# Performance work log

Measured on AMD Instinct MI355X. Metric: run time of the kernel, lower is better.

Reference implementation:

```python
import jax, jax.numpy as jnp
import numpy as np

EPS = 1e-5

def _layernorm(x, g, b):
    m = jnp.mean(x, axis=-1, keepdims=True)
    v = jnp.mean(jnp.square(x - m), axis=-1, keepdims=True)
    return (x - m) * jax.lax.rsqrt(v + EPS) * g + b

def setup_inputs() -> dict:
    key = jax.random.key(0)
    B, S, D, H = 2, 2048, 1024, 16
    F = 4 * D
    ks = jax.random.split(key, 12)
    s = 1.0 / np.sqrt(D)
    inp = {
        "x": jax.random.normal(ks[0], (B, S, D), dtype=jnp.float32),
        "mask": jnp.ones((B, S), dtype=jnp.int32),
        "wq": jax.random.normal(ks[1], (D, D), dtype=jnp.float32) * s,
        "bq": jnp.zeros((D,), jnp.float32),
        "wk": jax.random.normal(ks[2], (D, D), dtype=jnp.float32) * s,
        "bk": jnp.zeros((D,), jnp.float32),
        "wv": jax.random.normal(ks[3], (D, D), dtype=jnp.float32) * s,
        "bv": jnp.zeros((D,), jnp.float32),
        "wo": jax.random.normal(ks[4], (D, D), dtype=jnp.float32) * s,
        "bo": jnp.zeros((D,), jnp.float32),
        "g1": jnp.ones((D,), jnp.float32),
        "be1": jnp.zeros((D,), jnp.float32),
        "g2": jnp.ones((D,), jnp.float32),
        "be2": jnp.zeros((D,), jnp.float32),
        "w1": jax.random.normal(ks[5], (D, F), dtype=jnp.float32) * s,
        "bf1": jnp.zeros((F,), jnp.float32),
        "w2": jax.random.normal(ks[6], (F, D), dtype=jnp.float32) * (1.0 / np.sqrt(F)),
        "bf2": jnp.zeros((D,), jnp.float32),
    }
    return inp

def reference(x, mask, wq, bq, wk, bk, wv, bv, wo, bo, g1, be1, g2, be2, w1, bf1, w2, bf2):
    B, S, D = x.shape
    H = 16
    hd = D // H
    residual = x
    xn = _layernorm(x, g1, be1)
    q = (xn @ wq + bq).reshape(B, S, H, hd).transpose(0, 2, 1, 3)  # [B,H,S,hd]
    k = (xn @ wk + bk).reshape(B, S, H, hd).transpose(0, 2, 1, 3)
    v = (xn @ wv + bv).reshape(B, S, H, hd).transpose(0, 2, 1, 3)
    scores = jnp.einsum('bhqd,bhkd->bhqk', q, k) / np.sqrt(hd)  # [B,H,S,S]
    scores = jnp.where(mask[:, None, None, :] == 0, jnp.float32(-1e9), scores)
    attn = jax.nn.softmax(scores, axis=-1)
    attended = jnp.einsum('bhqk,bhkd->bhqd', attn, v)
    attended = attended.transpose(0, 2, 1, 3).reshape(B, S, D)
    x = residual + (attended @ wo + bo)
    residual = x
    xn = _layernorm(x, g2, be2)
    ff = jax.nn.relu(xn @ w1 + bf1) @ w2 + bf2
    return residual + ff
```

## Files before the change

kernel.cpp:

```cpp
#include <hip/hip_runtime.h>
#include <hip/hip_bf16.h>


using bf16 = __hip_bfloat16;
typedef short bf16x8 __attribute__((ext_vector_type(8)));
typedef short bf16x4v __attribute__((ext_vector_type(4)));
typedef float f32x4 __attribute__((ext_vector_type(4)));

#if defined(__has_builtin)
#  if __has_builtin(__builtin_amdgcn_mfma_f32_16x16x16bf16_1k)
#    define HAVE_MFMA_K16 1
#  endif
#  if __has_builtin(__builtin_amdgcn_exp2f)
#    define EXP2F(x) __builtin_amdgcn_exp2f(x)
#  endif
#endif
#ifndef EXP2F
#  define EXP2F(x) __expf(0.6931471805599453f * (x))
#endif

__device__ __forceinline__ float toF(float v) { return v; }
__device__ __forceinline__ float toF(bf16 v) { return __bfloat162float(v); }
__device__ __forceinline__ void storeF(float* p, float v) { *p = v; }
__device__ __forceinline__ void storeF(bf16* p, float v) { *p = __float2bfloat16(v); }

__device__ __forceinline__ float waveReduceSum(float v) {
    #pragma unroll
    for (int o = 32; o > 0; o >>= 1) v += __shfl_down(v, o, 64);
    return v;
}

__device__ __forceinline__ void async16(const bf16* g, bf16* l) {
    __builtin_amdgcn_global_load_lds(
        (const __attribute__((address_space(1))) unsigned int*)g,
        (__attribute__((address_space(3))) unsigned int*)l,
        16, 0, 0);
}

__device__ __forceinline__ unsigned short bf16bits(float x) {
    union { bf16 h; unsigned short u; } e; e.h = __float2bfloat16(x);
    return e.u;
}

__global__ __launch_bounds__(256) void transpose_all(
        const float* __restrict__ wq, const float* __restrict__ wk,
        const float* __restrict__ wv, const float* __restrict__ wo,
        const float* __restrict__ w1, const float* __restrict__ w2,
        bf16* __restrict__ wqkvT, bf16* __restrict__ woT,
        bf16* __restrict__ w1T, bf16* __restrict__ w2T) {
    __shared__ float t[32][33];
    const int tI = blockIdx.x;
    const float* in; bf16* outT; int R, C, tl;
    if (tI < 4096) {
        const int seg = tI >> 10; tl = tI & 1023; R = 1024; C = 1024;
        in = (seg == 0) ? wq : (seg == 1) ? wk : (seg == 2) ? wv : wo;
        outT = (seg == 3) ? woT : wqkvT + (size_t)seg * 1024 * 1024;
    } else if (tI < 8192) {
        tl = tI - 4096; in = w1; outT = w1T; R = 1024; C = 4096;
    } else {
        tl = tI - 8192; in = w2; outT = w2T; R = 4096; C = 1024;
    }
    const int tc = C >> 5;
    const int c0 = (tl % tc) * 32, r0 = (tl / tc) * 32;
    const int lx = threadIdx.x & 31, ly = threadIdx.x >> 5;
    #pragma unroll
    for (int i = 0; i < 32; i += 8)
        t[ly + i][lx] = in[(size_t)(r0 + ly + i) * C + c0 + lx];
    __syncthreads();
    #pragma unroll
    for (int i = 0; i < 32; i += 8)
        outT[(size_t)(c0 + ly + i) * R + r0 + lx] = __float2bfloat16(t[lx][ly + i]);
}

template <typename InT>
__global__ __launch_bounds__(256) void ln_kernel(const InT* __restrict__ x,
                                                 const float* __restrict__ g,
                                                 const float* __restrict__ b,
                                                 bf16* __restrict__ out, int D) {
    const int row = blockIdx.x;
    const InT* xr = x + (size_t)row * D;
    float s = 0.f, s2 = 0.f;
    for (int i = threadIdx.x; i < D; i += 256) {
        float v = toF(xr[i]);
        s += v; s2 += v * v;
    }
    __shared__ float ws[4], ws2[4];
    int lane = threadIdx.x & 63, wid = threadIdx.x >> 6;
    s = waveReduceSum(s); s2 = waveReduceSum(s2);
    if (lane == 0) { ws[wid] = s; ws2[wid] = s2; }
    __syncthreads();
    float ts = ws[0] + ws[1] + ws[2] + ws[3];
    float ts2 = ws2[0] + ws2[1] + ws2[2] + ws2[3];
    float mean = ts / D;
    float var = ts2 / D - mean * mean;
    float rstd = rsqrtf(var + 1e-5f);
    bf16* outr = out + (size_t)row * D;
    for (int i = threadIdx.x; i < D; i += 256) {
        float v = (toF(xr[i]) - mean) * rstd * g[i] + b[i];
        outr[i] = __float2bfloat16(v);
    }
}

template <int BM, typename OutT, typename ResidT, bool RELU, bool HAS_RESID, bool BIAS3>
__global__ __launch_bounds__(256) void gemm_mfma(const bf16* __restrict__ A,
                                                 const bf16* __restrict__ BT,
                                                 const float* __restrict__ bias,
                                                 const float* __restrict__ biasK,
                                                 const float* __restrict__ biasV,
                                                 const ResidT* __restrict__ resid,
                                                 OutT* __restrict__ C,
                                                 int M, int N, int K) {
    constexpr int BK = 64;
    constexpr int MI = BM / 32;
    constexpr int AROWS = BM / 4;
    constexpr int ASEC = AROWS / 8;
    __shared__ bf16 As[BM][BK];
    __shared__ bf16 Bs[128][BK];
    const int tid = threadIdx.x, lane = tid & 63, wid = tid >> 6;
    const int m0 = blockIdx.y * BM, n0 = blockIdx.x * 128;
    const int wm = (BM == 128) ? (wid >> 1) * 64 : (wid & 1) * 32;
    const int wn = (BM == 128) ? (wid & 1) * 64 : (wid >> 1) * 64;

    f32x4 acc[MI][4] = {};

    const int srow = lane >> 3;
    const int scol = ((lane & 7) ^ srow) * 8;
    const bf16* Abase = A + (size_t)(m0 + wid * AROWS + srow) * K + scol;
    const bf16* Bbase = BT + (size_t)(n0 + wid * 32 + srow) * K + scol;

    const int fr = lane & 15;
    const int kg = lane >> 4;

    for (int k0 = 0; k0 < K; k0 += BK) {
        #pragma unroll
        for (int s = 0; s < ASEC; ++s)
            async16(Abase + (size_t)(s * 8) * K + k0, &As[wid * AROWS + s * 8][0]);
        #pragma unroll
        for (int s = 0; s < 4; ++s)
            async16(Bbase + (size_t)(s * 8) * K + k0, &Bs[wid * 32 + s * 8][0]);
        __syncthreads();

        #pragma unroll
        for (int ks = 0; ks < 2; ++ks) {
            const int pc = ((ks * 4 + kg) ^ (fr & 7)) * 16;
            bf16x8 aF[MI], bF[4];
            #pragma unroll
            for (int i = 0; i < MI; ++i)
                aF[i] = *(const bf16x8*)((const char*)&As[0][0]
                         + (size_t)(wm + i * 16 + fr) * 128 + pc);
            #pragma unroll
            for (int j = 0; j < 4; ++j)
                bF[j] = *(const bf16x8*)((const char*)&Bs[0][0]
                         + (size_t)(wn + j * 16 + fr) * 128 + pc);
            #pragma unroll
            for (int i = 0; i < MI; ++i)
                #pragma unroll
                for (int j = 0; j < 4; ++j)
                    acc[i][j] = __builtin_amdgcn_mfma_f32_16x16x32_bf16(
                        aF[i], bF[j], acc[i][j], 0, 0, 0);
        }
        __syncthreads();
    }

    const int col_l = lane & 15, row_l = (lane >> 4) * 4;
    #pragma unroll
    for (int j = 0; j < 4; ++j) {
        const int col = n0 + wn + j * 16 + col_l;
        float bvv;
        if (BIAS3) {
            const float* bp = (col < 1024) ? bias : ((col < 2048) ? biasK : biasV);
            bvv = bp[col & 1023];
        } else {
            bvv = bias[col];
        }
        #pragma unroll
        for (int i = 0; i < MI; ++i) {
            #pragma unroll
            for (int r = 0; r < 4; ++r) {
                const int row = m0 + wm + i * 16 + row_l + r;
                float v = acc[i][j][r] + bvv;
                if (RELU) v = fmaxf(v, 0.f);
                if (HAS_RESID) v += toF(resid[(size_t)row * N + col]);
                storeF(&C[(size_t)row * N + col], v);
            }
        }
    }
}

#if HAVE_MFMA_K16
__global__ __launch_bounds__(256) void attn_mfma(const bf16* __restrict__ qkv,
                                                 const int* __restrict__ mask,
                                                 bf16* __restrict__ outp,
                                                 int B, int S, int LD) {
    const int q0 = blockIdx.x * 128;
    const int h = blockIdx.y, b = blockIdx.z;
    const int Do = 1024;
    const int tid = threadIdx.x, lane = tid & 63, wid = tid >> 6;
    const int n = lane & 15, kg = lane >> 4;

    __shared__ bf16 Ks[2][64][66];
    __shared__ bf16 Vt[2][64][68];
    __shared__ float Mskf[2][64];
    __shared__ int sAny[2];

    const float QSCALE = 0.125f * 1.4426950408889634f;
    bf16x8 qf[2][2];
    #pragma unroll
    for (int u = 0; u < 2; ++u) {
        const bf16* qp = qkv + ((size_t)(b * S + q0 + wid * 32 + u * 16 + n)) * LD + h * 64 + kg * 8;
        union { uint4 uu; bf16x8 v; unsigned short s[8]; } c[2];
        c[0].uu = *(const uint4*)qp;
        c[1].uu = *(const uint4*)(qp + 32);
        #pragma unroll
        for (int t = 0; t < 2; ++t) {
            #pragma unroll
            for (int i = 0; i < 8; ++i) {
                union { float f; unsigned int u2; } d;
                d.u2 = ((unsigned int)c[t].s[i]) << 16;
                c[t].s[i] = bf16bits(d.f * QSCALE);
            }
            qf[u][t] = c[t].v;
        }
    }

    f32x4 acc[2][4] = {};
    float m[2] = {-1e30f, -1e30f}, l[2] = {0.f, 0.f};

    const int sr = tid >> 2, sc = (tid & 3) * 16;
    const int jp = tid & 31, dg = (tid >> 5) * 8;
    const bf16* kbase = qkv + (size_t)(b * S) * LD + 1024 + h * 64;
    const bf16* vbase = qkv + (size_t)(b * S) * LD + 2048 + h * 64;

    uint4 ka, kc, vau, vcu;
    int mz = 0;

    {
        const bf16* kp = kbase + (size_t)sr * LD + sc;
        ka = *(const uint4*)kp;
        kc = *(const uint4*)(kp + 8);
        const bf16* vp = vbase + (size_t)(2 * jp) * LD + dg;
        vau = *(const uint4*)vp;
        vcu = *(const uint4*)(vp + LD);
        if (tid < 64) mz = (mask[b * S + tid] == 0);
    }

    const int NT = S / 64;
    for (int t = 0; t < NT; ++t) {
        const int cur = t & 1;

        {
            uint* kd = (uint*)((char*)&Ks[cur][0][0] + sr * 132 + sc * 2);
            kd[0] = ka.x; kd[1] = ka.y; kd[2] = ka.z; kd[3] = ka.w;
            kd[4] = kc.x; kd[5] = kc.y; kd[6] = kc.z; kd[7] = kc.w;

            union { uint4 u4; unsigned short s[8]; } va, vc;
            va.u4 = vau; vc.u4 = vcu;
            #pragma unroll
            for (int i = 0; i < 8; ++i) {
                unsigned int pk = (unsigned int)va.s[i] | ((unsigned int)vc.s[i] << 16);
                *(unsigned int*)((char*)&Vt[cur][0][0] + (size_t)(dg + i) * 136 + jp * 4) = pk;
            }
            if (tid < 64) {
                Mskf[cur][tid] = mz ? -1e9f : 0.f;
                unsigned long long bl = __ballot(mz);
                if (tid == 0) sAny[cur] = (bl != 0ull) ? 1 : 0;
            }
        }
        __syncthreads();

        if (t + 1 < NT) {
            const int j0 = (t + 1) * 64;
            const bf16* kp = kbase + (size_t)(j0 + sr) * LD + sc;
            ka = *(const uint4*)kp;
            kc = *(const uint4*)(kp + 8);
            const bf16* vp = vbase + (size_t)(j0 + 2 * jp) * LD + dg;
            vau = *(const uint4*)vp;
            vcu = *(const uint4*)(vp + LD);
            if (tid < 64) mz = (mask[b * S + j0 + tid] == 0);
        }

        f32x4 st[2][4] = {};
        #pragma unroll
        for (int ks = 0; ks < 2; ++ks) {
            #pragma unroll
            for (int jt = 0; jt < 4; ++jt) {
                union { uint u[4]; bf16x8 v; } kf;
                const uint* bp = (const uint*)((const char*)&Ks[cur][0][0]
                                 + (size_t)(jt * 16 + n) * 132 + ks * 64 + kg * 16);
                kf.u[0] = bp[0]; kf.u[1] = bp[1]; kf.u[2] = bp[2]; kf.u[3] = bp[3];
                st[0][jt] = __builtin_amdgcn_mfma_f32_16x16x32_bf16(kf.v, qf[0][ks], st[0][jt], 0, 0, 0);
                st[1][jt] = __builtin_amdgcn_mfma_f32_16x16x32_bf16(kf.v, qf[1][ks], st[1][jt], 0, 0, 0);
            }
        }

        if (sAny[cur]) {
            #pragma unroll
            for (int u = 0; u < 2; ++u) {
                #pragma unroll
                for (int jt = 0; jt < 4; ++jt) {
                    f32x4 mb = *(const f32x4*)&Mskf[cur][jt * 16 + kg * 4];
                    #pragma unroll
                    for (int r = 0; r < 4; ++r) st[u][jt][r] += mb[r];
                }
            }
        }

        float mx0 = st[0][0][0], mx1 = st[1][0][0];
        #pragma unroll
        for (int jt = 0; jt < 4; ++jt) {
            #pragma unroll
            for (int r = 0; r < 4; ++r) {
                mx0 = fmaxf(mx0, st[0][jt][r]);
                mx1 = fmaxf(mx1, st[1][jt][r]);
            }
        }
        mx0 = fmaxf(mx0, __shfl_xor(mx0, 16, 64));
        mx0 = fmaxf(mx0, __shfl_xor(mx0, 32, 64));
        mx1 = fmaxf(mx1, __shfl_xor(mx1, 16, 64));
        mx1 = fmaxf(mx1, __shfl_xor(mx1, 32, 64));

        if (__any((mx0 > m[0] + 8.f) || (mx1 > m[1] + 8.f))) {
            float mxa[2] = {mx0, mx1};
            #pragma unroll
            for (int u = 0; u < 2; ++u) {
                float newm = fmaxf(m[u], mxa[u]);
                float alpha = EXP2F(m[u] - newm);
                m[u] = newm;
                l[u] *= alpha;
                #pragma unroll
                for (int dt = 0; dt < 4; ++dt)
                    #pragma unroll
                    for (int r = 0; r < 4; ++r) acc[u][dt][r] *= alpha;
            }
        }

        bf16x4v pf[2][4];
        #pragma unroll
        for (int u = 0; u < 2; ++u) {
            float ls = 0.f;
            #pragma unroll
            for (int jt = 0; jt < 4; ++jt) {
                union { unsigned short s[4]; bf16x4v v; } pk;
                #pragma unroll
                for (int r = 0; r < 4; ++r) {
                    union { float f; unsigned int u2; } p;
                    p.f = EXP2F(st[u][jt][r] - m[u]);
                    p.u2 &= 0xffff0000u;
                    ls += p.f;
                    pk.s[r] = (unsigned short)(p.u2 >> 16);
                }
                pf[u][jt] = pk.v;
            }
            ls += __shfl_xor(ls, 16, 64);
            ls += __shfl_xor(ls, 32, 64);
            l[u] += ls;
        }

        #pragma unroll
        for (int jt = 0; jt < 4; ++jt) {
            #pragma unroll
            for (int dt = 0; dt < 4; ++dt) {
                union { uint u[2]; bf16x4v v; } vf;
                const uint* vpp = (const uint*)((const char*)&Vt[cur][0][0]
                                  + (size_t)(dt * 16 + n) * 136 + jt * 32 + kg * 8);
                vf.u[0] = vpp[0]; vf.u[1] = vpp[1];
                acc[0][dt] = __builtin_amdgcn_mfma_f32_16x16x16bf16_1k(vf.v, pf[0][jt], acc[0][dt], 0, 0, 0);
                acc[1][dt] = __builtin_amdgcn_mfma_f32_16x16x16bf16_1k(vf.v, pf[1][jt], acc[1][dt], 0, 0, 0);
            }
        }
    }

    #pragma unroll
    for (int u = 0; u < 2; ++u) {
        float inv = (l[u] > 0.f) ? (1.f / l[u]) : 0.f;
        bf16* op = outp + ((size_t)(b * S + q0 + wid * 32 + u * 16 + n)) * Do + h * 64;
        #pragma unroll
        for (int dt = 0; dt < 4; ++dt) {
            union { unsigned short s[4]; uint2 u2; } w;
            #pragma unroll
            for (int r = 0; r < 4; ++r) w.s[r] = bf16bits(acc[u][dt][r] * inv);
            *(uint2*)(op + dt * 16 + kg * 4) = w.u2;
        }
    }
}
#else
__global__ __launch_bounds__(256) void attn_mfma(const bf16* __restrict__ qkv,
                                                 const int* __restrict__ mask,
                                                 bf16* __restrict__ outp,
                                                 int B, int S, int LD) {
    const int h = blockIdx.y, b = blockIdx.z;
    const int Do = 1024;
    const int tid = threadIdx.x, lane = tid & 63, wid = tid >> 6;
    const int n = lane & 15, kg = lane >> 4;

    __shared__ bf16 Ks[64][66];
    __shared__ bf16 Vt[64][66];
    __shared__ bf16 Plds[4][16][66];
    __shared__ int  Msk[64];

    for (int half = 0; half < 2; ++half) {
        const int q0 = blockIdx.x * 128 + half * 64;
        __syncthreads();

        bf16x8 qf[2];
        {
            const bf16* qp = qkv + ((size_t)(b * S + q0 + wid * 16 + n)) * LD + h * 64 + kg * 8;
            union { uint4 u; bf16x8 v; } c0, c1;
            c0.u = *(const uint4*)qp;
            c1.u = *(const uint4*)(qp + 32);
            qf[0] = c0.v; qf[1] = c1.v;
        }

        f32x4 acc_o[4] = {};
        float m_r[4] = {-1e30f, -1e30f, -1e30f, -1e30f};
        float l_r[4] = {0.f, 0.f, 0.f, 0.f};

        const int sr = tid >> 2;
        const int sc = (tid & 3) * 16;
        const bf16* kbase = qkv + (size_t)(b * S) * LD + 1024 + h * 64;
        const bf16* vbase = qkv + (size_t)(b * S) * LD + 2048 + h * 64;

        for (int j0 = 0; j0 < S; j0 += 64) {
            __syncthreads();
            {
                const bf16* kp = kbase + (size_t)(j0 + sr) * LD + sc;
                uint4 ka = *(const uint4*)kp;
                uint4 kbv = *(const uint4*)(kp + 8);
                uint* kd = (uint*)((char*)&Ks[0][0] + sr * 132 + sc * 2);
                kd[0] = ka.x; kd[1] = ka.y; kd[2] = ka.z; kd[3] = ka.w;
                kd[4] = kbv.x; kd[5] = kbv.y; kd[6] = kbv.z; kd[7] = kbv.w;

                const bf16* vp = vbase + (size_t)(j0 + sr) * LD + sc;
                union { uint4 u[2]; unsigned short s[16]; } vv;
                vv.u[0] = *(const uint4*)vp;
                vv.u[1] = *(const uint4*)(vp + 8);
                #pragma unroll
                for (int i = 0; i < 16; ++i)
                    *((unsigned short*)((char*)&Vt[0][0] + (size_t)(sc + i) * 132 + sr * 2)) = vv.s[i];

                if (tid < 64) Msk[tid] = mask[b * S + j0 + tid];
            }
            __syncthreads();

            f32x4 st[4] = {};
            #pragma unroll
            for (int ks = 0; ks < 2; ++ks) {
                #pragma unroll
                for (int jt = 0; jt < 4; ++jt) {
                    union { uint u[4]; bf16x8 v; } bf;
                    const uint* bp = (const uint*)((const char*)&Ks[0][0]
                                     + (size_t)(jt * 16 + n) * 132 + ks * 64 + kg * 16);
                    bf.u[0] = bp[0]; bf.u[1] = bp[1]; bf.u[2] = bp[2]; bf.u[3] = bp[3];
                    st[jt] = __builtin_amdgcn_mfma_f32_16x16x32_bf16(qf[ks], bf.v, st[jt], 0, 0, 0);
                }
            }

            int mk[4];
            #pragma unroll
            for (int jt = 0; jt < 4; ++jt) mk[jt] = Msk[jt * 16 + n];

            #pragma unroll
            for (int r = 0; r < 4; ++r) {
                float mx = -1e30f;
                #pragma unroll
                for (int jt = 0; jt < 4; ++jt) {
                    float s = st[jt][r] * 0.125f;
                    if (mk[jt] == 0) s = -1e9f;
                    st[jt][r] = s;
                    mx = fmaxf(mx, s);
                }
                #pragma unroll
                for (int o = 1; o < 16; o <<= 1) mx = fmaxf(mx, __shfl_xor(mx, o, 64));
                float newm = fmaxf(m_r[r], mx);
                float alpha = __expf(m_r[r] - newm);
                m_r[r] = newm;
                float ls = 0.f;
                #pragma unroll
                for (int jt = 0; jt < 4; ++jt) {
                    float p = __expf(st[jt][r] - newm);
                    ls += p;
                    Plds[wid][kg * 4 + r][jt * 16 + n] = __float2bfloat16(p);
                }
                #pragma unroll
                for (int o = 1; o < 16; o <<= 1) ls += __shfl_xor(ls, o, 64);
                l_r[r] = l_r[r] * alpha + ls;
                #pragma unroll
                for (int dt = 0; dt < 4; ++dt) acc_o[dt][r] *= alpha;
            }

            __asm__ volatile("s_waitcnt lgkmcnt(0)" ::: "memory");

            #pragma unroll
            for (int ks = 0; ks < 2; ++ks) {
                union { uint u[4]; bf16x8 v; } af;
                const uint* ap = (const uint*)((const char*)&Plds[wid][0][0]
                                 + (size_t)n * 132 + ks * 64 + kg * 16);
                af.u[0] = ap[0]; af.u[1] = ap[1]; af.u[2] = ap[2]; af.u[3] = ap[3];
                #pragma unroll
                for (int dt = 0; dt < 4; ++dt) {
                    union { uint u[4]; bf16x8 v; } bf;
                    const uint* bp = (const uint*)((const char*)&Vt[0][0]
                                     + (size_t)(dt * 16 + n) * 132 + ks * 64 + kg * 16);
                    bf.u[0] = bp[0]; bf.u[1] = bp[1]; bf.u[2] = bp[2]; bf.u[3] = bp[3];
                    acc_o[dt] = __builtin_amdgcn_mfma_f32_16x16x32_bf16(af.v, bf.v, acc_o[dt], 0, 0, 0);
                }
            }
        }

        #pragma unroll
        for (int r = 0; r < 4; ++r) {
            float inv = (l_r[r] > 0.f) ? (1.f / l_r[r]) : 0.f;
            bf16* op = outp + ((size_t)(b * S + q0 + wid * 16 + kg * 4 + r)) * Do + h * 64 + n;
            #pragma unroll
            for (int dt = 0; dt < 4; ++dt)
                op[dt * 16] = __float2bfloat16(acc_o[dt][r] * inv);
        }
    }
}
#endif

extern "C" void kernel_launch(void* const* d_in, const int* in_sizes, int n_in,
                              void* d_out, int out_size, void* d_ws, size_t ws_size,
                              hipStream_t stream) {
    const int B = 2, S = 2048, D = 1024, H = 16, F = 4096;
    const int M = B * S;

    const float* x   = (const float*)d_in[0];
    const int*   mask= (const int*)  d_in[1];
    const float* wq  = (const float*)d_in[2];
    const float* bq  = (const float*)d_in[3];
    const float* wk  = (const float*)d_in[4];
    const float* bk  = (const float*)d_in[5];
    const float* wv  = (const float*)d_in[6];
    const float* bv  = (const float*)d_in[7];
    const float* wo  = (const float*)d_in[8];
    const float* bo  = (const float*)d_in[9];
    const float* g1  = (const float*)d_in[10];
    const float* be1 = (const float*)d_in[11];
    const float* g2  = (const float*)d_in[12];
    const float* be2 = (const float*)d_in[13];
    const float* w1  = (const float*)d_in[14];
    const float* bf1 = (const float*)d_in[15];
    const float* w2  = (const float*)d_in[16];
    const float* bf2 = (const float*)d_in[17];
    float* out = (float*)d_out;

    char* ws = (char*)d_ws;
    const size_t MB = 1024 * 1024;
    bf16* wqkvT = (bf16*)(ws + 0 * MB);
    bf16* woT   = (bf16*)(ws + 6 * MB);
    bf16* w1T   = (bf16*)(ws + 8 * MB);
    bf16* w2T   = (bf16*)(ws + 16 * MB);
    bf16* xn    = (bf16*)(ws + 24 * MB);
    bf16* qkv   = (bf16*)(ws + 32 * MB);
    bf16* att   = xn;

    const bool fullM = (ws_size >= 64 * MB);

    transpose_all<<<12288, 256, 0, stream>>>(wq, wk, wv, wo, w1, w2,
                                             wqkvT, woT, w1T, w2T);

    ln_kernel<float><<<M, 256, 0, stream>>>(x, g1, be1, xn, D);

    gemm_mfma<128, bf16, float, false, false, true><<<dim3(3072 / 128, M / 128), 256, 0, stream>>>(
        xn, wqkvT, bq, bk, bv, (const float*)nullptr, qkv, M, 3072, D);

    attn_mfma<<<dim3(S / 128, H, B), 256, 0, stream>>>(qkv, mask, att, B, S, 3072);

    gemm_mfma<64, float, float, false, true, false><<<dim3(D / 128, M / 64), 256, 0, stream>>>(
        att, woT, bo, nullptr, nullptr, x, out, M, D, D);

    if (fullM) {
        bf16* hid = (bf16*)(ws + 24 * MB);
        bf16* xn2 = (bf16*)(ws + 56 * MB);
        ln_kernel<float><<<M, 256, 0, stream>>>(out, g2, be2, xn2, D);
        gemm_mfma<128, bf16, float, true, false, false><<<dim3(F / 128, M / 128), 256, 0, stream>>>(
            xn2, w1T, bf1, nullptr, nullptr, (const float*)nullptr, hid, M, F, D);
        gemm_mfma<64, float, float, false, true, false><<<dim3(D / 128, M / 64), 256, 0, stream>>>(
            hid, w2T, bf2, nullptr, nullptr, out, out, M, D, F);
    } else {
        bf16* xn2 = (bf16*)(ws + 32 * MB);
        bf16* hid = (bf16*)(ws + 40 * MB);
        const int CH = 2048;
        ln_kernel<float><<<M, 256, 0, stream>>>(out, g2, be2, xn2, D);
        for (int c = 0; c < M / CH; ++c) {
            const size_t roff = (size_t)c * CH;
            gemm_mfma<128, bf16, float, true, false, false><<<dim3(F / 128, CH / 128), 256, 0, stream>>>(
                xn2 + roff * D, w1T, bf1, nullptr, nullptr, (const float*)nullptr, hid, CH, F, D);
            gemm_mfma<64, float, float, false, true, false><<<dim3(D / 128, CH / 64), 256, 0, stream>>>(
                hid, w2T, bf2, nullptr, nullptr, out + roff * D, out + roff * D, CH, D, F);
        }
    }
}
```

Measured before the change: 392.2 us.

## Split attention KV sequence across two wave groups and merge partial softmax

The attention kernel now launches 512 threads per block, split into two groups of four waves. Each group processes alternating 64-key tiles for the same 128 queries with its own double-buffered LDS slots. At the end, the partial max, sum and output of group 1 are merged into group 0 through shared memory. The aim is to add parallelism and hide latency, since the grid has only 512 blocks. The cost is about 70KB of LDS per block, which limits occupancy, plus an extra merge step.

```diff
diff --git a/kernel.cpp b/kernel.cpp
--- a/kernel.cpp
+++ b/kernel.cpp
@@ -188,26 +188,30 @@
 }
 
 #if HAVE_MFMA_K16
-__global__ __launch_bounds__(256) void attn_mfma(const bf16* __restrict__ qkv,
-                                                 const int* __restrict__ mask,
-                                                 bf16* __restrict__ outp,
-                                                 int B, int S, int LD) {
+__global__ __launch_bounds__(512, 4) void attn_mfma(const bf16* __restrict__ qkv,
+                                                    const int* __restrict__ mask,
+                                                    bf16* __restrict__ outp,
+                                                    int B, int S, int LD) {
     const int q0 = blockIdx.x * 128;
     const int h = blockIdx.y, b = blockIdx.z;
     const int Do = 1024;
     const int tid = threadIdx.x, lane = tid & 63, wid = tid >> 6;
+    const int g = wid >> 2;
+    const int wl = wid & 3;
+    const int stid = tid & 255;
     const int n = lane & 15, kg = lane >> 4;
 
-    __shared__ bf16 Ks[2][64][66];
-    __shared__ bf16 Vt[2][64][68];
-    __shared__ float Mskf[2][64];
-    __shared__ int sAny[2];
+    __shared__ __align__(16) char smem[70672];
+    bf16* KsBase = (bf16*)smem;
+    bf16* VtBase = (bf16*)(smem + 33792);
+    float* MskfP = (float*)(smem + 68608);
+    int* sAnyP   = (int*)(smem + 70656);
 
     const float QSCALE = 0.125f * 1.4426950408889634f;
     bf16x8 qf[2][2];
     #pragma unroll
     for (int u = 0; u < 2; ++u) {
-        const bf16* qp = qkv + ((size_t)(b * S + q0 + wid * 32 + u * 16 + n)) * LD + h * 64 + kg * 8;
+        const bf16* qp = qkv + ((size_t)(b * S + q0 + wl * 32 + u * 16 + n)) * LD + h * 64 + kg * 8;
         union { uint4 uu; bf16x8 v; unsigned short s[8]; } c[2];
         c[0].uu = *(const uint4*)qp;
         c[1].uu = *(const uint4*)(qp + 32);
@@ -226,8 +230,8 @@
     f32x4 acc[2][4] = {};
     float m[2] = {-1e30f, -1e30f}, l[2] = {0.f, 0.f};
 
-    const int sr = tid >> 2, sc = (tid & 3) * 16;
-    const int jp = tid & 31, dg = (tid >> 5) * 8;
+    const int sr = stid >> 2, sc = (stid & 3) * 16;
+    const int jp = stid & 31, dg = (stid >> 5) * 8;
     const bf16* kbase = qkv + (size_t)(b * S) * LD + 1024 + h * 64;
     const bf16* vbase = qkv + (size_t)(b * S) * LD + 2048 + h * 64;
 
@@ -235,21 +239,25 @@
     int mz = 0;
 
     {
-        const bf16* kp = kbase + (size_t)sr * LD + sc;
+        const int j0 = g * 64;
+        const bf16* kp = kbase + (size_t)(j0 + sr) * LD + sc;
         ka = *(const uint4*)kp;
         kc = *(const uint4*)(kp + 8);
-        const bf16* vp = vbase + (size_t)(2 * jp) * LD + dg;
+        const bf16* vp = vbase + (size_t)(j0 + 2 * jp) * LD + dg;
         vau = *(const uint4*)vp;
         vcu = *(const uint4*)(vp + LD);
-        if (tid < 64) mz = (mask[b * S + tid] == 0);
+        if (stid < 64) mz = (mask[b * S + j0 + stid] == 0);
     }
 
     const int NT = S / 64;
-    for (int t = 0; t < NT; ++t) {
-        const int cur = t & 1;
+    for (int it = 0; it < NT / 2; ++it) {
+        const int cur = it & 1;
+        const int slot = g * 2 + cur;
+        bf16* ksb = KsBase + slot * (64 * 66);
+        bf16* vtb = VtBase + slot * (64 * 68);
 
         {
-            uint* kd = (uint*)((char*)&Ks[cur][0][0] + sr * 132 + sc * 2);
+            uint* kd = (uint*)((char*)ksb + sr * 132 + sc * 2);
             kd[0] = ka.x; kd[1] = ka.y; kd[2] = ka.z; kd[3] = ka.w;
             kd[4] = kc.x; kd[5] = kc.y; kd[6] = kc.z; kd[7] = kc.w;
 
@@ -258,25 +266,28 @@
             #pragma unroll
             for (int i = 0; i < 8; ++i) {
                 unsigned int pk = (unsigned int)va.s[i] | ((unsigned int)vc.s[i] << 16);
-                *(unsigned int*)((char*)&Vt[cur][0][0] + (size_t)(dg + i) * 136 + jp * 4) = pk;
-            }
-            if (tid < 64) {
-                Mskf[cur][tid] = mz ? -1e9f : 0.f;
+                *(unsigned int*)((char*)vtb + (size_t)(dg + i) * 136 + jp * 4) = pk;
+            }
+            if (stid < 64) {
+                MskfP[slot * 64 + stid] = mz ? -1e9f : 0.f;
                 unsigned long long bl = __ballot(mz);
-                if (tid == 0) sAny[cur] = (bl != 0ull) ? 1 : 0;
+                if (stid == 0) sAnyP[slot] = (bl != 0ull) ? 1 : 0;
             }
         }
         __syncthreads();
 
-        if (t + 1 < NT) {
-            const int j0 = (t + 1) * 64;
-            const bf16* kp = kbase + (size_t)(j0 + sr) * LD + sc;
-            ka = *(const uint4*)kp;
-            kc = *(const uint4*)(kp + 8);
-            const bf16* vp = vbase + (size_t)(j0 + 2 * jp) * LD + dg;
-            vau = *(const uint4*)vp;
-            vcu = *(const uint4*)(vp + LD);
-            if (tid < 64) mz = (mask[b * S + j0 + tid] == 0);
+        {
+            const int tg2 = 2 * (it + 1) + g;
+            if (tg2 < NT) {
+                const int j0 = tg2 * 64;
+                const bf16* kp = kbase + (size_t)(j0 + sr) * LD + sc;
+                ka = *(const uint4*)kp;
+                kc = *(const uint4*)(kp + 8);
+                const bf16* vp = vbase + (size_t)(j0 + 2 * jp) * LD + dg;
+                vau = *(const uint4*)vp;
+                vcu = *(const uint4*)(vp + LD);
+                if (stid < 64) mz = (mask[b * S + j0 + stid] == 0);
+            }
         }
 
         f32x4 st[2][4] = {};
@@ -285,7 +296,7 @@
             #pragma unroll
             for (int jt = 0; jt < 4; ++jt) {
                 union { uint u[4]; bf16x8 v; } kf;
-                const uint* bp = (const uint*)((const char*)&Ks[cur][0][0]
+                const uint* bp = (const uint*)((const char*)ksb
                                  + (size_t)(jt * 16 + n) * 132 + ks * 64 + kg * 16);
                 kf.u[0] = bp[0]; kf.u[1] = bp[1]; kf.u[2] = bp[2]; kf.u[3] = bp[3];
                 st[0][jt] = __builtin_amdgcn_mfma_f32_16x16x32_bf16(kf.v, qf[0][ks], st[0][jt], 0, 0, 0);
@@ -293,12 +304,12 @@
             }
         }
 
-        if (sAny[cur]) {
+        if (sAnyP[slot]) {
             #pragma unroll
             for (int u = 0; u < 2; ++u) {
                 #pragma unroll
                 for (int jt = 0; jt < 4; ++jt) {
-                    f32x4 mb = *(const f32x4*)&Mskf[cur][jt * 16 + kg * 4];
+                    f32x4 mb = *(const f32x4*)&MskfP[slot * 64 + jt * 16 + kg * 4];
                     #pragma unroll
                     for (int r = 0; r < 4; ++r) st[u][jt][r] += mb[r];
                 }
@@ -361,7 +372,7 @@
             #pragma unroll
             for (int dt = 0; dt < 4; ++dt) {
                 union { uint u[2]; bf16x4v v; } vf;
-                const uint* vpp = (const uint*)((const char*)&Vt[cur][0][0]
+                const uint* vpp = (const uint*)((const char*)vtb
                                   + (size_t)(dt * 16 + n) * 136 + jt * 32 + kg * 8);
                 vf.u[0] = vpp[0]; vf.u[1] = vpp[1];
                 acc[0][dt] = __builtin_amdgcn_mfma_f32_16x16x16bf16_1k(vf.v, pf[0][jt], acc[0][dt], 0, 0, 0);
@@ -370,21 +381,49 @@
         }
     }
 
-    #pragma unroll
-    for (int u = 0; u < 2; ++u) {
-        float inv = (l[u] > 0.f) ? (1.f / l[u]) : 0.f;
-        bf16* op = outp + ((size_t)(b * S + q0 + wid * 32 + u * 16 + n)) * Do + h * 64;
-        #pragma unroll
-        for (int dt = 0; dt < 4; ++dt) {
-            union { unsigned short s[4]; uint2 u2; } w;
-            #pragma unroll
-            for (int r = 0; r < 4; ++r) w.s[r] = bf16bits(acc[u][dt][r] * inv);
-            *(uint2*)(op + dt * 16 + kg * 4) = w.u2;
+    __syncthreads();
+    float* po = (float*)smem;
+    float* pm = (float*)(smem + 33280);
+    float* pl = (float*)(smem + 33792);
+    if (g == 1) {
+        #pragma unroll
+        for (int u = 0; u < 2; ++u) {
+            const int ql = wl * 32 + u * 16 + n;
+            if (kg == 0) { pm[ql] = m[u]; pl[ql] = l[u]; }
+            #pragma unroll
+            for (int dt = 0; dt < 4; ++dt)
+                #pragma unroll
+                for (int r = 0; r < 4; ++r)
+                    po[ql * 65 + dt * 16 + kg * 4 + r] = acc[u][dt][r];
+        }
+    }
+    __syncthreads();
+    if (g == 0) {
+        #pragma unroll
+        for (int u = 0; u < 2; ++u) {
+            const int ql = wl * 32 + u * 16 + n;
+            float m1 = pm[ql], l1 = pl[ql];
+            float newm = fmaxf(m[u], m1);
+            float a0 = EXP2F(m[u] - newm);
+            float a1 = EXP2F(m1 - newm);
+            float lt = l[u] * a0 + l1 * a1;
+            float inv = (lt > 0.f) ? (1.f / lt) : 0.f;
+            bf16* op = outp + ((size_t)(b * S + q0 + wl * 32 + u * 16 + n)) * Do + h * 64;
+            #pragma unroll
+            for (int dt = 0; dt < 4; ++dt) {
+                union { unsigned short s[4]; uint2 u2; } w;
+                #pragma unroll
+                for (int r = 0; r < 4; ++r) {
+                    float o1 = po[ql * 65 + dt * 16 + kg * 4 + r];
+                    w.s[r] = bf16bits((acc[u][dt][r] * a0 + o1 * a1) * inv);
+                }
+                *(uint2*)(op + dt * 16 + kg * 4) = w.u2;
+            }
         }
     }
 }
 #else
-__global__ __launch_bounds__(256) void attn_mfma(const bf16* __restrict__ qkv,
+__global__ __launch_bounds__(512) void attn_mfma(const bf16* __restrict__ qkv,
                                                  const int* __restrict__ mask,
                                                  bf16* __restrict__ outp,
                                                  int B, int S, int LD) {
@@ -392,129 +431,125 @@
     const int Do = 1024;
     const int tid = threadIdx.x, lane = tid & 63, wid = tid >> 6;
     const int n = lane & 15, kg = lane >> 4;
+    const int q0 = blockIdx.x * 128;
 
     __shared__ bf16 Ks[64][66];
     __shared__ bf16 Vt[64][66];
-    __shared__ bf16 Plds[4][16][66];
+    __shared__ bf16 Plds[8][16][66];
     __shared__ int  Msk[64];
 
-    for (int half = 0; half < 2; ++half) {
-        const int q0 = blockIdx.x * 128 + half * 64;
+    bf16x8 qf[2];
+    {
+        const bf16* qp = qkv + ((size_t)(b * S + q0 + wid * 16 + n)) * LD + h * 64 + kg * 8;
+        union { uint4 u; bf16x8 v; } c0, c1;
+        c0.u = *(const uint4*)qp;
+        c1.u = *(const uint4*)(qp + 32);
+        qf[0] = c0.v; qf[1] = c1.v;
+    }
+
+    f32x4 acc_o[4] = {};
+    float m_r[4] = {-1e30f, -1e30f, -1e30f, -1e30f};
+    float l_r[4] = {0.f, 0.f, 0.f, 0.f};
+
+    const int sr = tid >> 2;
+    const int sc = (tid & 3) * 16;
+    const bf16* kbase = qkv + (size_t)(b * S) * LD + 1024 + h * 64;
+    const bf16* vbase = qkv + (size_t)(b * S) * LD + 2048 + h * 64;
+
+    for (int j0 = 0; j0 < S; j0 += 64) {
         __syncthreads();
-
-        bf16x8 qf[2];
-        {
-            const bf16* qp = qkv + ((size_t)(b * S + q0 + wid * 16 + n)) * LD + h * 64 + kg * 8;
-            union { uint4 u; bf16x8 v; } c0, c1;
-            c0.u = *(const uint4*)qp;
-            c1.u = *(const uint4*)(qp + 32);
-            qf[0] = c0.v; qf[1] = c1.v;
-        }
-
-        f32x4 acc_o[4] = {};
-        float m_r[4] = {-1e30f, -1e30f, -1e30f, -1e30f};
-        float l_r[4] = {0.f, 0.f, 0.f, 0.f};
-
-        const int sr = tid >> 2;
-        const int sc = (tid & 3) * 16;
-        const bf16* kbase = qkv + (size_t)(b * S) * LD + 1024 + h * 64;
-        const bf16* vbase = qkv + (size_t)(b * S) * LD + 2048 + h * 64;
-
-        for (int j0 = 0; j0 < S; j0 += 64) {
-            __syncthreads();
-            {
-                const bf16* kp = kbase + (size_t)(j0 + sr) * LD + sc;
-                uint4 ka = *(const uint4*)kp;
-                uint4 kbv = *(const uint4*)(kp + 8);
-                uint* kd = (uint*)((char*)&Ks[0][0] + sr * 132 + sc * 2);
-                kd[0] = ka.x; kd[1] = ka.y; kd[2] = ka.z; kd[3] = ka.w;
-                kd[4] = kbv.x; kd[5] = kbv.y; kd[6] = kbv.z; kd[7] = kbv.w;
-
-                const bf16* vp = vbase + (size_t)(j0 + sr) * LD + sc;
-                union { uint4 u[2]; unsigned short s[16]; } vv;
-                vv.u[0] = *(const uint4*)vp;
-                vv.u[1] = *(const uint4*)(vp + 8);
-                #pragma unroll
-                for (int i = 0; i < 16; ++i)
-                    *((unsigned short*)((char*)&Vt[0][0] + (size_t)(sc + i) * 132 + sr * 2)) = vv.s[i];
-
-                if (tid < 64) Msk[tid] = mask[b * S + j0 + tid];
-            }
-            __syncthreads();
-
-            f32x4 st[4] = {};
-            #pragma unroll
-            for (int ks = 0; ks < 2; ++ks) {
-                #pragma unroll
-                for (int jt = 0; jt < 4; ++jt) {
-                    union { uint u[4]; bf16x8 v; } bf;
-                    const uint* bp = (const uint*)((const char*)&Ks[0][0]
-                                     + (size_t)(jt * 16 + n) * 132 + ks * 64 + kg * 16);
-                    bf.u[0] = bp[0]; bf.u[1] = bp[1]; bf.u[2] = bp[2]; bf.u[3] = bp[3];
-                    st[jt] = __builtin_amdgcn_mfma_f32_16x16x32_bf16(qf[ks], bf.v, st[jt], 0, 0, 0);
-                }
-            }
-
-            int mk[4];
-            #pragma unroll
-            for (int jt = 0; jt < 4; ++jt) mk[jt] = Msk[jt * 16 + n];
-
-            #pragma unroll
-            for (int r = 0; r < 4; ++r) {
-                float mx = -1e30f;
-                #pragma unroll
-                for (int jt = 0; jt < 4; ++jt) {
-                    float s = st[jt][r] * 0.125f;
-                    if (mk[jt] == 0) s = -1e9f;
-                    st[jt][r] = s;
-                    mx = fmaxf(mx, s);
-                }
-                #pragma unroll
-                for (int o = 1; o < 16; o <<= 1) mx = fmaxf(mx, __shfl_xor(mx, o, 64));
-                float newm = fmaxf(m_r[r], mx);
-                float alpha = __expf(m_r[r] - newm);
-                m_r[r] = newm;
-                float ls = 0.f;
-                #pragma unroll
-                for (int jt = 0; jt < 4; ++jt) {
-                    float p = __expf(st[jt][r] - newm);
-                    ls += p;
-                    Plds[wid][kg * 4 + r][jt * 16 + n] = __float2bfloat16(p);
-                }
-                #pragma unroll
-                for (int o = 1; o < 16; o <<= 1) ls += __shfl_xor(ls, o, 64);
-                l_r[r] = l_r[r] * alpha + ls;
-                #pragma unroll
-                for (int dt = 0; dt < 4; ++dt) acc_o[dt][r] *= alpha;
-            }
-
-            __asm__ volatile("s_waitcnt lgkmcnt(0)" ::: "memory");
-
-            #pragma unroll
-            for (int ks = 0; ks < 2; ++ks) {
-                union { uint u[4]; bf16x8 v; } af;
-                const uint* ap = (const uint*)((const char*)&Plds[wid][0][0]
-                                 + (size_t)n * 132 + ks * 64 + kg * 16);
-                af.u[0] = ap[0]; af.u[1] = ap[1]; af.u[2] = ap[2]; af.u[3] = ap[3];
-                #pragma unroll
-                for (int dt = 0; dt < 4; ++dt) {
-                    union { uint u[4]; bf16x8 v; } bf;
-                    const uint* bp = (const uint*)((const char*)&Vt[0][0]
-                                     + (size_t)(dt * 16 + n) * 132 + ks * 64 + kg * 16);
-                    bf.u[0] = bp[0]; bf.u[1] = bp[1]; bf.u[2] = bp[2]; bf.u[3] = bp[3];
-                    acc_o[dt] = __builtin_amdgcn_mfma_f32_16x16x32_bf16(af.v, bf.v, acc_o[dt], 0, 0, 0);
-                }
-            }
-        }
+        if (tid < 256) {
+            const bf16* kp = kbase + (size_t)(j0 + sr) * LD + sc;
+            uint4 ka = *(const uint4*)kp;
+            uint4 kbv = *(const uint4*)(kp + 8);
+            uint* kd = (uint*)((char*)&Ks[0][0] + sr * 132 + sc * 2);
+            kd[0] = ka.x; kd[1] = ka.y; kd[2] = ka.z; kd[3] = ka.w;
+            kd[4] = kbv.x; kd[5] = kbv.y; kd[6] = kbv.z; kd[7] = kbv.w;
+
+            const bf16* vp = vbase + (size_t)(j0 + sr) * LD + sc;
+            union { uint4 u[2]; unsigned short s[16]; } vv;
+            vv.u[0] = *(const uint4*)vp;
+            vv.u[1] = *(const uint4*)(vp + 8);
+            #pragma unroll
+            for (int i = 0; i < 16; ++i)
+                *((unsigned short*)((char*)&Vt[0][0] + (size_t)(sc + i) * 132 + sr * 2)) = vv.s[i];
+
+            if (tid < 64) Msk[tid] = mask[b * S + j0 + tid];
+        }
+        __syncthreads();
+
+        f32x4 st[4] = {};
+        #pragma unroll
+        for (int ks = 0; ks < 2; ++ks) {
+            #pragma unroll
+            for (int jt = 0; jt < 4; ++jt) {
+                union { uint u[4]; bf16x8 v; } bf;
+                const uint* bp = (const uint*)((const char*)&Ks[0][0]
+                                 + (size_t)(jt * 16 + n) * 132 + ks * 64 + kg * 16);
+                bf.u[0] = bp[0]; bf.u[1] = bp[1]; bf.u[2] = bp[2]; bf.u[3] = bp[3];
+                st[jt] = __builtin_amdgcn_mfma_f32_16x16x32_bf16(qf[ks], bf.v, st[jt], 0, 0, 0);
+            }
+        }
+
+        int mk[4];
+        #pragma unroll
+        for (int jt = 0; jt < 4; ++jt) mk[jt] = Msk[jt * 16 + n];
 
         #pragma unroll
         for (int r = 0; r < 4; ++r) {
-            float inv = (l_r[r] > 0.f) ? (1.f / l_r[r]) : 0.f;
-            bf16* op = outp + ((size_t)(b * S + q0 + wid * 16 + kg * 4 + r)) * Do + h * 64 + n;
-            #pragma unroll
-            for (int dt = 0; dt < 4; ++dt)
-                op[dt * 16] = __float2bfloat16(acc_o[dt][r] * inv);
-        }
+            float mx = -1e30f;
+            #pragma unroll
+            for (int jt = 0; jt < 4; ++jt) {
+                float s = st[jt][r] * 0.125f;
+                if (mk[jt] == 0) s = -1e9f;
+                st[jt][r] = s;
+                mx = fmaxf(mx, s);
+            }
+            #pragma unroll
+            for (int o = 1; o < 16; o <<= 1) mx = fmaxf(mx, __shfl_xor(mx, o, 64));
+            float newm = fmaxf(m_r[r], mx);
+            float alpha = __expf(m_r[r] - newm);
+            m_r[r] = newm;
+            float ls = 0.f;
+            #pragma unroll
+            for (int jt = 0; jt < 4; ++jt) {
+                float p = __expf(st[jt][r] - newm);
+                ls += p;
+                Plds[wid][kg * 4 + r][jt * 16 + n] = __float2bfloat16(p);
+            }
+            #pragma unroll
+            for (int o = 1; o < 16; o <<= 1) ls += __shfl_xor(ls, o, 64);
+            l_r[r] = l_r[r] * alpha + ls;
+            #pragma unroll
+            for (int dt = 0; dt < 4; ++dt) acc_o[dt][r] *= alpha;
+        }
+
+        __asm__ volatile("s_waitcnt lgkmcnt(0)" ::: "memory");
+
+        #pragma unroll
+        for (int ks = 0; ks < 2; ++ks) {
+            union { uint u[4]; bf16x8 v; } af;
+            const uint* ap = (const uint*)((const char*)&Plds[wid][0][0]
+                             + (size_t)n * 132 + ks * 64 + kg * 16);
+            af.u[0] = ap[0]; af.u[1] = ap[1]; af.u[2] = ap[2]; af.u[3] = ap[3];
+            #pragma unroll
+            for (int dt = 0; dt < 4; ++dt) {
+                union { uint u[4]; bf16x8 v; } bf;
+                const uint* bp = (const uint*)((const char*)&Vt[0][0]
+                                 + (size_t)(dt * 16 + n) * 132 + ks * 64 + kg * 16);
+                bf.u[0] = bp[0]; bf.u[1] = bp[1]; bf.u[2] = bp[2]; bf.u[3] = bp[3];
+                acc_o[dt] = __builtin_amdgcn_mfma_f32_16x16x32_bf16(af.v, bf.v, acc_o[dt], 0, 0, 0);
+            }
+        }
+    }
+
+    #pragma unroll
+    for (int r = 0; r < 4; ++r) {
+        float inv = (l_r[r] > 0.f) ? (1.f / l_r[r]) : 0.f;
+        bf16* op = outp + ((size_t)(b * S + q0 + wid * 16 + kg * 4 + r)) * Do + h * 64 + n;
+        #pragma unroll
+        for (int dt = 0; dt < 4; ++dt)
+            op[dt * 16] = __float2bfloat16(acc_o[dt][r] * inv);
     }
 }
 #endif
@@ -565,7 +600,7 @@
     gemm_mfma<128, bf16, float, false, false, true><<<dim3(3072 / 128, M / 128), 256, 0, stream>>>(
         xn, wqkvT, bq, bk, bv, (const float*)nullptr, qkv, M, 3072, D);
 
-    attn_mfma<<<dim3(S / 128, H, B), 256, 0, stream>>>(qkv, mask, att, B, S, 3072);
+    attn_mfma<<<dim3(S / 128, H, B), 512, 0, stream>>>(qkv, mask, att, B, S, 3072);
 
     gemm_mfma<64, float, float, false, true, false><<<dim3(D / 128, M / 64), 256, 0, stream>>>(
         att, woT, bo, nullptr, nullptr, x, out, M, D, D);
```

Result: slower. 406.7 us (+3.7%).

## Add 256x256-tile 8-wave MFMA GEMM for FFN up-projection

Applied to the files above, without the earlier changes.

Adds a new GEMM kernel using 256x256 output tiles with 512 threads, double-buffered async global-to-LDS loads with XOR swizzle, and 16x16x32 bf16 MFMA interleaved with split prefetches, barriers, and priority raises. It replaces the 128-tile GEMM for the W1+ReLU FFN projection only in the full-M path. The larger tile is meant to increase operand reuse and the scheduling to overlap loads with MFMA. In exchange it raises register and LDS use (one block per CU) and yields fewer blocks (16x16=256 tiles), which could hurt wave occupancy and load balance.

```diff
diff --git a/kernel.cpp b/kernel.cpp
--- a/kernel.cpp
+++ b/kernel.cpp
@@ -14,9 +14,21 @@
 #  if __has_builtin(__builtin_amdgcn_exp2f)
 #    define EXP2F(x) __builtin_amdgcn_exp2f(x)
 #  endif
+#  if __has_builtin(__builtin_amdgcn_sched_barrier)
+#    define SCHED_BARRIER() __builtin_amdgcn_sched_barrier(0)
+#  endif
+#  if __has_builtin(__builtin_amdgcn_s_setprio)
+#    define SETPRIO(x) __builtin_amdgcn_s_setprio(x)
+#  endif
 #endif
 #ifndef EXP2F
 #  define EXP2F(x) __expf(0.6931471805599453f * (x))
+#endif
+#ifndef SCHED_BARRIER
+#  define SCHED_BARRIER()
+#endif
+#ifndef SETPRIO
+#  define SETPRIO(x)
 #endif
 
 __device__ __forceinline__ float toF(float v) { return v; }
@@ -187,6 +199,163 @@
     }
 }
 
+template <bool RELU>
+__global__ __launch_bounds__(512, 1) void gemm_mfma256(const bf16* __restrict__ A,
+                                                       const bf16* __restrict__ BT,
+                                                       const float* __restrict__ bias,
+                                                       bf16* __restrict__ C,
+                                                       int M, int N, int K) {
+    constexpr int BK = 64;
+    __shared__ bf16 As[2][256][BK];
+    __shared__ bf16 Bs[2][256][BK];
+    const int tid = threadIdx.x, lane = tid & 63, wid = tid >> 6;
+    const int m0 = blockIdx.y * 256, n0 = blockIdx.x * 256;
+    const int wm = (wid >> 2) * 128, wn = (wid & 3) * 64;
+
+    f32x4 acc[8][4] = {};
+
+    const int srow = lane >> 3;
+    const int scol = ((lane & 7) ^ srow) * 8;
+    const bf16* Abase = A + (size_t)(m0 + wid * 16 + srow) * K + scol;
+    const bf16* Bbase = BT + (size_t)(n0 + wid * 16 + srow) * K + scol;
+
+    const int fr = lane & 15;
+    const int kg = lane >> 4;
+    const int NT = K / BK;
+
+    #pragma unroll
+    for (int h = 0; h < 2; ++h)
+        #pragma unroll
+        for (int s = 0; s < 2; ++s) {
+            async16(Abase + (size_t)(h * 128 + s * 8) * K,
+                    &As[0][h * 128 + wid * 16 + s * 8][0]);
+            async16(Bbase + (size_t)(h * 128 + s * 8) * K,
+                    &Bs[0][h * 128 + wid * 16 + s * 8][0]);
+        }
+    asm volatile("s_waitcnt vmcnt(0)" ::: "memory");
+    __builtin_amdgcn_s_barrier();
+    SCHED_BARRIER();
+
+    for (int t = 0; t < NT; ++t) {
+        const int cur = t & 1;
+        const size_t k1 = (size_t)(t + 1) * BK;
+        const char* ab = (const char*)&As[cur][0][0];
+        const char* bb = (const char*)&Bs[cur][0][0];
+        const bool pf = (t + 1 < NT);
+        bf16x8 aF[4][2], bF[4][2];
+
+        #pragma unroll
+        for (int i = 0; i < 4; ++i)
+            #pragma unroll
+            for (int kk = 0; kk < 2; ++kk)
+                aF[i][kk] = *(const bf16x8*)(ab + (size_t)(wm + i * 16 + fr) * 128
+                                             + ((kk * 4 + kg) ^ (fr & 7)) * 16);
+        #pragma unroll
+        for (int j = 0; j < 2; ++j)
+            #pragma unroll
+            for (int kk = 0; kk < 2; ++kk)
+                bF[j][kk] = *(const bf16x8*)(bb + (size_t)(wn + j * 16 + fr) * 128
+                                             + ((kk * 4 + kg) ^ (fr & 7)) * 16);
+        if (pf) {
+            #pragma unroll
+            for (int h = 0; h < 2; ++h)
+                #pragma unroll
+                for (int s = 0; s < 2; ++s)
+                    async16(Abase + (size_t)(h * 128 + s * 8) * K + k1,
+                            &As[cur ^ 1][h * 128 + wid * 16 + s * 8][0]);
+        }
+        __builtin_amdgcn_s_barrier();
+        SCHED_BARRIER();
+        SETPRIO(1);
+        #pragma unroll
+        for (int i = 0; i < 4; ++i)
+            #pragma unroll
+            for (int j = 0; j < 2; ++j)
+                #pragma unroll
+                for (int kk = 0; kk < 2; ++kk)
+                    acc[i][j] = __builtin_amdgcn_mfma_f32_16x16x32_bf16(
+                        aF[i][kk], bF[j][kk], acc[i][j], 0, 0, 0);
+        SETPRIO(0);
+
+        #pragma unroll
+        for (int j = 2; j < 4; ++j)
+            #pragma unroll
+            for (int kk = 0; kk < 2; ++kk)
+                bF[j][kk] = *(const bf16x8*)(bb + (size_t)(wn + j * 16 + fr) * 128
+                                             + ((kk * 4 + kg) ^ (fr & 7)) * 16);
+        if (pf) {
+            #pragma unroll
+            for (int h = 0; h < 2; ++h)
+                #pragma unroll
+                for (int s = 0; s < 2; ++s)
+                    async16(Bbase + (size_t)(h * 128 + s * 8) * K + k1,
+                            &Bs[cur ^ 1][h * 128 + wid * 16 + s * 8][0]);
+        }
+        __builtin_amdgcn_s_barrier();
+        SCHED_BARRIER();
+        SETPRIO(1);
+        #pragma unroll
+        for (int i = 0; i < 4; ++i)
+            #pragma unroll
+            for (int j = 2; j < 4; ++j)
+                #pragma unroll
+                for (int kk = 0; kk < 2; ++kk)
+                    acc[i][j] = __builtin_amdgcn_mfma_f32_16x16x32_bf16(
+                        aF[i][kk], bF[j][kk], acc[i][j], 0, 0, 0);
+        SETPRIO(0);
+
+        #pragma unroll
+        for (int i = 0; i < 4; ++i)
+            #pragma unroll
+            for (int kk = 0; kk < 2; ++kk)
+                aF[i][kk] = *(const bf16x8*)(ab + (size_t)(wm + (i + 4) * 16 + fr) * 128
+                                             + ((kk * 4 + kg) ^ (fr & 7)) * 16);
+        __builtin_amdgcn_s_barrier();
+        SCHED_BARRIER();
+        SETPRIO(1);
+        #pragma unroll
+        for (int i = 0; i < 4; ++i)
+            #pragma unroll
+            for (int j = 0; j < 2; ++j)
+                #pragma unroll
+                for (int kk = 0; kk < 2; ++kk)
+                    acc[i + 4][j] = __builtin_amdgcn_mfma_f32_16x16x32_bf16(
+                        aF[i][kk], bF[j][kk], acc[i + 4][j], 0, 0, 0);
+        SETPRIO(0);
+
+        if (pf) asm volatile("s_waitcnt vmcnt(0)" ::: "memory");
+        __builtin_amdgcn_s_barrier();
+        SCHED_BARRIER();
+        SETPRIO(1);
+        #pragma unroll
+        for (int i = 0; i < 4; ++i)
+            #pragma unroll
+            for (int j = 2; j < 4; ++j)
+                #pragma unroll
+                for (int kk = 0; kk < 2; ++kk)
+                    acc[i + 4][j] = __builtin_amdgcn_mfma_f32_16x16x32_bf16(
+                        aF[i][kk], bF[j][kk], acc[i + 4][j], 0, 0, 0);
+        SETPRIO(0);
+    }
+
+    const int col_l = lane & 15, row_l = (lane >> 4) * 4;
+    #pragma unroll
+    for (int j = 0; j < 4; ++j) {
+        const int col = n0 + wn + j * 16 + col_l;
+        const float bvv = bias[col];
+        #pragma unroll
+        for (int i = 0; i < 8; ++i) {
+            #pragma unroll
+            for (int r = 0; r < 4; ++r) {
+                const int row = m0 + wm + i * 16 + row_l + r;
+                float v = acc[i][j][r] + bvv;
+                if (RELU) v = fmaxf(v, 0.f);
+                C[(size_t)row * N + col] = __float2bfloat16(v);
+            }
+        }
+    }
+}
+
 #if HAVE_MFMA_K16
 __global__ __launch_bounds__(256) void attn_mfma(const bf16* __restrict__ qkv,
                                                  const int* __restrict__ mask,
@@ -574,8 +743,8 @@
         bf16* hid = (bf16*)(ws + 24 * MB);
         bf16* xn2 = (bf16*)(ws + 56 * MB);
         ln_kernel<float><<<M, 256, 0, stream>>>(out, g2, be2, xn2, D);
-        gemm_mfma<128, bf16, float, true, false, false><<<dim3(F / 128, M / 128), 256, 0, stream>>>(
-            xn2, w1T, bf1, nullptr, nullptr, (const float*)nullptr, hid, M, F, D);
+        gemm_mfma256<true><<<dim3(F / 256, M / 256), 512, 0, stream>>>(
+            xn2, w1T, bf1, hid, M, F, D);
         gemm_mfma<64, float, float, false, true, false><<<dim3(D / 128, M / 64), 256, 0, stream>>>(
             hid, w2T, bf2, nullptr, nullptr, out, out, M, D, F);
     } else {
```

After: 387.5 us. About the same (-1.2%).
